# Kernel optimization log

Measured on AMD Instinct MI355X. Metric: run time of the kernel, lower is better.

Reference implementation:

```python
import jax, jax.numpy as jnp
import numpy as np

N = 200000
D_NODE = 256
D_EDGE = 128
D_OUT = 256
J = 17


def setup_inputs() -> dict:
    key = jax.random.key(0)
    ks = jax.random.split(key, 16)
    s = 0.02
    return {
        "nodes_1": jax.random.normal(ks[0], (N, D_NODE), jnp.float32),
        "nodes_2": jax.random.normal(ks[1], (N, D_NODE), jnp.float32),
        "edges": jax.random.normal(ks[2], (N, D_EDGE), jnp.float32),
        "node_types_1": jax.random.randint(ks[3], (N,), 0, J),
        "node_types_2": jax.random.randint(ks[4], (N,), 0, J),
        # per-joint linear stacks (torch Linear weight [out,in] stored transposed as [in,out])
        "W1": jax.random.normal(ks[5], (J, D_NODE, D_OUT), jnp.float32) * s,
        "b1": jax.random.normal(ks[6], (J, D_OUT), jnp.float32) * s,
        "W2": jax.random.normal(ks[7], (J, D_NODE, D_OUT), jnp.float32) * s,
        "b2": jax.random.normal(ks[8], (J, D_OUT), jnp.float32) * s,
        "We": jax.random.normal(ks[9], (D_EDGE, D_OUT), jnp.float32) * s,
        "be": jax.random.normal(ks[10], (D_OUT,), jnp.float32) * s,
        "Wout": jax.random.normal(ks[11], (3 * D_OUT, D_OUT), jnp.float32) * s,
        "bout": jax.random.normal(ks[12], (D_OUT,), jnp.float32) * s,
    }


def _per_type_linear(nodes, types, W, b):
    # Equivalent to: for each joint i, tmp[types==i] = nodes[types==i] @ W[i] + b[i]
    out = jnp.zeros((nodes.shape[0], W.shape[2]), nodes.dtype)
    for i in range(W.shape[0]):  # small fixed loop over joint types
        yi = nodes @ W[i] + b[i]
        out = jnp.where((types == i)[:, None], yi, out)
    return out


def reference(nodes_1, nodes_2, edges, node_types_1, node_types_2,
              W1, b1, W2, b2, We, be, Wout, bout):
    tmp_1 = _per_type_linear(nodes_1, node_types_1, W1, b1)
    tmp_2 = _per_type_linear(nodes_2, node_types_2, W2, b2)
    e = edges @ We + be
    cat = jnp.concatenate([tmp_1, tmp_2, e], axis=1)  # [N, 3*D_OUT]
    h = jax.nn.relu(cat) @ Wout + bout
    return jax.nn.relu(h)
```

## Files before the change

kernel.cpp:

```cpp
#include <hip/hip_runtime.h>


#define J_TYPES 17
#define PAIRS   (J_TYPES * J_TYPES)
#define DN      256
#define DE      128
#define DO      256
#define TILE    64
#define LDA     264
#define LDE     136

typedef short bf16x8 __attribute__((ext_vector_type(8)));
typedef float f32x4  __attribute__((ext_vector_type(4)));

#define BAR() asm volatile("s_waitcnt lgkmcnt(0)\n\ts_barrier" ::: "memory")

__device__ __forceinline__ unsigned short f2bf(float x) {
  unsigned u = __float_as_uint(x);
  return (unsigned short)((u + 0x7fffu + ((u >> 16) & 1u)) >> 16);
}

__device__ __forceinline__ unsigned cvtpk(float lo, float hi) {
  unsigned r;
  asm("v_cvt_pk_bf16_f32 %0, %1, %2" : "=v"(r) : "v"(lo), "v"(hi));
  return r;
}

__global__ void prep_w_k(const float* __restrict__ W1, const float* __restrict__ W2,
                         const float* __restrict__ We, const float* __restrict__ Wout,
                         unsigned short* __restrict__ W1t, unsigned short* __restrict__ W2t,
                         unsigned short* __restrict__ Wet, unsigned short* __restrict__ Ut) {
  const int SZW = J_TYPES * 65536;
  const int total = SZW * 2 + DE * DO + 3 * 65536;
  for (int o = blockIdx.x * blockDim.x + threadIdx.x; o < total;
       o += gridDim.x * blockDim.x) {
    int idx = o;
    if (idx < SZW) {
      int j = idx >> 16, r = idx & 65535;
      int i = r & 7, lane = (r >> 3) & 63, t = r >> 9;
      int k32 = t & 7, colt = t >> 3;
      int col = colt * 16 + (lane & 15);
      int k = k32 * 32 + ((lane >> 4) << 3) + i;
      W1t[idx] = f2bf(W1[((size_t)j * 256 + k) * 256 + col]);
    } else if ((idx -= SZW) < SZW) {
      int j = idx >> 16, r = idx & 65535;
      int i = r & 7, lane = (r >> 3) & 63, t = r >> 9;
      int k32 = t & 7, colt = t >> 3;
      int col = colt * 16 + (lane & 15);
      int k = k32 * 32 + ((lane >> 4) << 3) + i;
      W2t[idx] = f2bf(W2[((size_t)j * 256 + k) * 256 + col]);
    } else if ((idx -= SZW) < DE * DO) {
      int r = idx;
      int i = r & 7, lane = (r >> 3) & 63, t = r >> 9;
      int k32 = t & 3, colt = t >> 2;
      int col = colt * 16 + (lane & 15);
      int k = k32 * 32 + ((lane >> 4) << 3) + i;
      Wet[idx] = f2bf(We[(size_t)k * 256 + col]);
    } else {
      idx -= DE * DO;
      int p = idx >> 16, r = idx & 65535;
      int i = r & 7, lane = (r >> 3) & 63, t = r >> 9;
      int k32 = t & 7, colt = t >> 3;
      int col = colt * 16 + (lane & 15);
      int k = k32 * 32 + ((lane >> 4) << 3) + i;
      Ut[idx] = f2bf(Wout[((size_t)p * 256 + k) * 256 + col]);
    }
  }
}

__global__ void hist_k(const int* __restrict__ ty1, const int* __restrict__ ty2,
                       int* __restrict__ cnt, int N) {
  __shared__ int h[PAIRS];
  for (int i = threadIdx.x; i < PAIRS; i += blockDim.x) h[i] = 0;
  __syncthreads();
  for (int i = blockIdx.x * blockDim.x + threadIdx.x; i < N;
       i += gridDim.x * blockDim.x)
    atomicAdd(&h[ty1[i] * J_TYPES + ty2[i]], 1);
  __syncthreads();
  for (int i = threadIdx.x; i < PAIRS; i += blockDim.x) {
    int v = h[i];
    if (v) atomicAdd(&cnt[i], v);
  }
}

__global__ void scan_tiles_k(const int* __restrict__ cnt, int* __restrict__ seg,
                             int* __restrict__ tpair, int* __restrict__ tstart,
                             int* __restrict__ tnr, int* __restrict__ ntl) {
  __shared__ int s1[512], s2[512];
  int t = threadIdx.x;
  int c  = (t < PAIRS) ? cnt[t] : 0;
  int nt = (c + TILE - 1) / TILE;
  s1[t] = c; s2[t] = nt;
  __syncthreads();
  for (int o = 1; o < 512; o <<= 1) {
    int v1 = (t >= o) ? s1[t - o] : 0;
    int v2 = (t >= o) ? s2[t - o] : 0;
    __syncthreads();
    s1[t] += v1; s2[t] += v2;
    __syncthreads();
  }
  if (t < PAIRS) {
    int segstart = s1[t] - c;
    int tbase    = s2[t] - nt;
    seg[t] = segstart;
    for (int i = 0; i < nt; ++i) {
      tpair[tbase + i]  = t;
      tstart[tbase + i] = segstart + i * TILE;
      int rem = c - i * TILE;
      tnr[tbase + i] = rem < TILE ? rem : TILE;
    }
  }
  if (t == 511) ntl[0] = s2[511];
}

__global__ void scatter_k(const int* __restrict__ ty1, const int* __restrict__ ty2,
                          const int* __restrict__ seg, int* __restrict__ c2,
                          int* __restrict__ ridx, int N) {
  __shared__ int lh[PAIRS], lb[PAIRS];
  int chunk = (N + gridDim.x - 1) / gridDim.x;
  int lo = blockIdx.x * chunk;
  int hi = lo + chunk; if (hi > N) hi = N;
  for (int i = threadIdx.x; i < PAIRS; i += blockDim.x) lh[i] = 0;
  __syncthreads();
  for (int i = lo + threadIdx.x; i < hi; i += blockDim.x)
    atomicAdd(&lh[ty1[i] * J_TYPES + ty2[i]], 1);
  __syncthreads();
  for (int i = threadIdx.x; i < PAIRS; i += blockDim.x) {
    int v = lh[i];
    lb[i] = v ? atomicAdd(&c2[i], v) : 0;
    lh[i] = 0;
  }
  __syncthreads();
  for (int i = lo + threadIdx.x; i < hi; i += blockDim.x) {
    int p = ty1[i] * J_TYPES + ty2[i];
    int pos = seg[p] + lb[p] + atomicAdd(&lh[p], 1);
    ridx[pos] = i;
  }
}


__device__ __forceinline__ void stage256(const float* __restrict__ src,
                                         const int* __restrict__ ridxp, int nrows,
                                         unsigned short* lds, int wave, int lane) {
  float4 f[8];
#pragma unroll
  for (int j = 0; j < 8; ++j) {
    int r = wave + 8 * j;
    int rc = r < nrows ? r : nrows - 1;
    int sr = ridxp[rc];
    f[j] = reinterpret_cast<const float4*>(src + (size_t)sr * DN)[lane];
  }
#pragma unroll
  for (int j = 0; j < 8; ++j) {
    int r = wave + 8 * j;
    unsigned lo = cvtpk(f[j].x, f[j].y), hi = cvtpk(f[j].z, f[j].w);
    *reinterpret_cast<uint2*>(lds + r * LDA + lane * 4) = make_uint2(lo, hi);
  }
}

__device__ __forceinline__ void stage128(const float* __restrict__ src,
                                         const int* __restrict__ ridxp, int nrows,
                                         unsigned short* lds, int wave, int lane) {
  float2 f[8];
#pragma unroll
  for (int j = 0; j < 8; ++j) {
    int r = wave + 8 * j;
    int rc = r < nrows ? r : nrows - 1;
    int sr = ridxp[rc];
    f[j] = reinterpret_cast<const float2*>(src + (size_t)sr * DE)[lane];
  }
#pragma unroll
  for (int j = 0; j < 8; ++j) {
    int r = wave + 8 * j;
    *reinterpret_cast<unsigned*>(lds + r * LDE + lane * 2) = cvtpk(f[j].x, f[j].y);
  }
}

template <int NK, int LD>
__device__ __forceinline__ void gemm32(const unsigned short* lds,
                                       const unsigned short* __restrict__ Wbase,
                                       f32x4 acc[4][2], int r0, int kg, int lane,
                                       int wave) {
  const unsigned short* w = Wbase + ((size_t)(wave * 2) * NK) * 512 + lane * 8;
  const int kw = wave & (NK - 1);
  bf16x8 bf[2][2];
#pragma unroll
  for (int cs = 0; cs < 2; ++cs)
    bf[0][cs] = *reinterpret_cast<const bf16x8*>(w + ((size_t)cs * NK + kw) * 512);
#pragma unroll
  for (int i = 0; i < NK; ++i) {
    const int cur = i & 1, nxt = cur ^ 1;
    const int kk = (i + wave) & (NK - 1);
    if (i + 1 < NK) {
      const int kk1 = (i + 1 + wave) & (NK - 1);
#pragma unroll
      for (int cs = 0; cs < 2; ++cs)
        bf[nxt][cs] =
            *reinterpret_cast<const bf16x8*>(w + ((size_t)cs * NK + kk1) * 512);
    }
    bf16x8 af[4];
#pragma unroll
    for (int rs = 0; rs < 4; ++rs)
      af[rs] = *reinterpret_cast<const bf16x8*>(lds + (rs * 16 + r0) * LD + kk * 32 + kg);
    __builtin_amdgcn_s_setprio(1);
#pragma unroll
    for (int rs = 0; rs < 4; ++rs)
#pragma unroll
      for (int cs = 0; cs < 2; ++cs)
        acc[rs][cs] = __builtin_amdgcn_mfma_f32_16x16x32_bf16(af[rs], bf[cur][cs],
                                                              acc[rs][cs], 0, 0, 0);
    __builtin_amdgcn_s_setprio(0);
  }
}

__device__ __forceinline__ void epi32(f32x4 accT[4][2], const float* __restrict__ bias,
                                      unsigned short* ldsT, int r0, int rb, int wave) {
#pragma unroll
  for (int cs = 0; cs < 2; ++cs) {
    int col = wave * 32 + cs * 16 + r0;
    float b = bias[col];
#pragma unroll
    for (int rs = 0; rs < 4; ++rs) {
      float x0 = fmaxf(accT[rs][cs][0] + b, 0.f);
      float x1 = fmaxf(accT[rs][cs][1] + b, 0.f);
      float x2 = fmaxf(accT[rs][cs][2] + b, 0.f);
      float x3 = fmaxf(accT[rs][cs][3] + b, 0.f);
      unsigned w01 = cvtpk(x0, x1), w23 = cvtpk(x2, x3);
      int row = rs * 16 + rb;
      ldsT[(row + 0) * LDA + col] = (unsigned short)w01;
      ldsT[(row + 1) * LDA + col] = (unsigned short)(w01 >> 16);
      ldsT[(row + 2) * LDA + col] = (unsigned short)w23;
      ldsT[(row + 3) * LDA + col] = (unsigned short)(w23 >> 16);
    }
  }
}

#define ZERO42(A)                                                        \
  _Pragma("unroll") for (int a_ = 0; a_ < 4; ++a_) _Pragma("unroll")     \
      for (int b_ = 0; b_ < 2; ++b_) A[a_][b_] = (f32x4){0.f, 0.f, 0.f, 0.f};

__global__ __launch_bounds__(512, 4) void fused_k(
    const float* __restrict__ n1, const float* __restrict__ n2,
    const float* __restrict__ eg, const unsigned short* __restrict__ W1t,
    const unsigned short* __restrict__ W2t, const unsigned short* __restrict__ Wet,
    const unsigned short* __restrict__ Ut, const float* __restrict__ b1,
    const float* __restrict__ b2, const float* __restrict__ be,
    const float* __restrict__ bout, const int* __restrict__ ridx,
    const int* __restrict__ tpair, const int* __restrict__ tstart,
    const int* __restrict__ tnr, const int* __restrict__ ntl,
    float* __restrict__ out) {
  int nwg = gridDim.x, orig = blockIdx.x;
  int q = nwg >> 3, rr = nwg & 7, xc = orig & 7, sidx = orig >> 3;
  int tile = (xc < rr ? xc * (q + 1) : rr * (q + 1) + (xc - rr) * q) + sidx;
  if (tile >= ntl[0]) return;

  const int pr = tpair[tile];
  const int t1 = pr / J_TYPES, t2 = pr % J_TYPES;
  const int ts = tstart[tile];
  const int nrows = tnr[tile];
  const int* __restrict__ ridxp = ridx + ts;

  __shared__ unsigned short ldsA[TILE * LDA];
  __shared__ unsigned short ldsT[TILE * LDA];
  __shared__ int srow[TILE];

  const int lane = threadIdx.x & 63;
  const int wave = __builtin_amdgcn_readfirstlane(threadIdx.x >> 6);
  const int r0 = lane & 15;
  const int kg = (lane >> 4) * 8;
  const int rb = (lane >> 4) * 4;

  if (threadIdx.x < TILE)
    srow[threadIdx.x] = (threadIdx.x < nrows) ? ridxp[threadIdx.x] : -1;

  f32x4 accT[4][2], accO[4][2];

  stage256(n1, ridxp, nrows, ldsA, wave, lane);
  BAR();

  ZERO42(accT);
  gemm32<8, LDA>(ldsA, W1t + (size_t)t1 * 65536, accT, r0, kg, lane, wave);
  BAR();

  epi32(accT, b1 + t1 * 256, ldsT, r0, rb, wave);
  stage256(n2, ridxp, nrows, ldsA, wave, lane);
  BAR();

  ZERO42(accO);
  gemm32<8, LDA>(ldsT, Ut, accO, r0, kg, lane, wave);
  ZERO42(accT);
  gemm32<8, LDA>(ldsA, W2t + (size_t)t2 * 65536, accT, r0, kg, lane, wave);
  BAR();

  epi32(accT, b2 + t2 * 256, ldsT, r0, rb, wave);
  stage128(eg, ridxp, nrows, ldsA, wave, lane);
  BAR();

  gemm32<8, LDA>(ldsT, Ut + 65536, accO, r0, kg, lane, wave);
  ZERO42(accT);
  gemm32<4, LDE>(ldsA, Wet, accT, r0, kg, lane, wave);
  BAR();

  epi32(accT, be, ldsT, r0, rb, wave);
  BAR();

  gemm32<8, LDA>(ldsT, Ut + 2 * 65536, accO, r0, kg, lane, wave);

#pragma unroll
  for (int cs = 0; cs < 2; ++cs) {
    int col = wave * 32 + cs * 16 + r0;
    float bo = bout[col];
#pragma unroll
    for (int rs = 0; rs < 4; ++rs)
#pragma unroll
      for (int i = 0; i < 4; ++i) {
        int row = rs * 16 + rb + i;
        if (row < nrows) {
          float v = fmaxf(accO[rs][cs][i] + bo, 0.f);
          out[(size_t)srow[row] * 256 + col] = v;
        }
      }
  }
}

extern "C" void kernel_launch(void* const* d_in, const int* in_sizes, int n_in,
                              void* d_out, int out_size, void* d_ws, size_t ws_size,
                              hipStream_t stream) {
  const float* n1   = (const float*)d_in[0];
  const float* n2   = (const float*)d_in[1];
  const float* eg   = (const float*)d_in[2];
  const int*   ty1  = (const int*)d_in[3];
  const int*   ty2  = (const int*)d_in[4];
  const float* W1   = (const float*)d_in[5];
  const float* b1   = (const float*)d_in[6];
  const float* W2   = (const float*)d_in[7];
  const float* b2   = (const float*)d_in[8];
  const float* We   = (const float*)d_in[9];
  const float* be   = (const float*)d_in[10];
  const float* Wout = (const float*)d_in[11];
  const float* bout = (const float*)d_in[12];
  float* out = (float*)d_out;

  const int N = in_sizes[0] / DN;
  const int maxt = (N + TILE - 1) / TILE + PAIRS;

  char* ws = (char*)d_ws;
  size_t off = 0;
  auto take = [&](size_t bytes) -> char* {
    char* p = ws + off;
    off += (bytes + 255) & ~(size_t)255;
    return p;
  };
  int* cnt = (int*)take(PAIRS * 4);
  int* c2  = (int*)take(PAIRS * 4);
  int* ntl = (int*)take(4);
  int* seg = (int*)take((PAIRS + 1) * 4);
  int* tp  = (int*)take((size_t)maxt * 4);
  int* tst = (int*)take((size_t)maxt * 4);
  int* tnr = (int*)take((size_t)maxt * 4);
  int* ridx = (int*)take((size_t)N * 4);
  unsigned short* W1t = (unsigned short*)take((size_t)J_TYPES * 65536 * 2);
  unsigned short* W2t = (unsigned short*)take((size_t)J_TYPES * 65536 * 2);
  unsigned short* Wet = (unsigned short*)take((size_t)DE * DO * 2);
  unsigned short* Ut  = (unsigned short*)take((size_t)3 * 65536 * 2);
  (void)ws_size; (void)n_in; (void)out_size;

  hipMemsetAsync(cnt, 0, (size_t)((char*)seg - (char*)cnt), stream);
  prep_w_k<<<1024, 256, 0, stream>>>(W1, W2, We, Wout, W1t, W2t, Wet, Ut);
  hist_k<<<400, 256, 0, stream>>>(ty1, ty2, cnt, N);
  scan_tiles_k<<<1, 512, 0, stream>>>(cnt, seg, tp, tst, tnr, ntl);
  scatter_k<<<256, 256, 0, stream>>>(ty1, ty2, seg, c2, ridx, N);
  fused_k<<<maxt, 512, 0, stream>>>(n1, n2, eg, W1t, W2t, Wet, Ut, b1, b2, be, bout,
                                    ridx, tp, tst, tnr, ntl, out);
}
```

Before: 289.5 us.

## Double-buffer input staging and split tile across 16 waves with 16-column slices

Moves the fused kernel from 512 to 1024 threads, so each of 16 waves computes a 16-column output slice instead of a 32-column one. Input row gathers are split into issue and LDS-write phases, and ldsA is double-buffered so the next input's global loads are in flight during the current GEMM. This is meant to hide gather latency and raise wave-level parallelism. In exchange it adds LDS use per block (an extra 64x264 bf16 buffer) and pairs 1024-thread blocks with launch_bounds(1024,4), which may constrain registers and occupancy.

After: 669.8 us. 131% more time.

```diff
diff --git a/kernel.cpp b/kernel.cpp
--- a/kernel.cpp
+++ b/kernel.cpp
@@ -139,64 +139,65 @@
 }
 
 
-__device__ __forceinline__ void stage256(const float* __restrict__ src,
+__device__ __forceinline__ void issue256(const float* __restrict__ src,
                                          const int* __restrict__ ridxp, int nrows,
-                                         unsigned short* lds, int wave, int lane) {
-  float4 f[8];
-#pragma unroll
-  for (int j = 0; j < 8; ++j) {
-    int r = wave + 8 * j;
+                                         int wave, int lane, float4 f[4]) {
+#pragma unroll
+  for (int j = 0; j < 4; ++j) {
+    int r = wave + 16 * j;
     int rc = r < nrows ? r : nrows - 1;
     int sr = ridxp[rc];
     f[j] = reinterpret_cast<const float4*>(src + (size_t)sr * DN)[lane];
   }
-#pragma unroll
-  for (int j = 0; j < 8; ++j) {
-    int r = wave + 8 * j;
+}
+
+__device__ __forceinline__ void write256(const float4 f[4], unsigned short* lds,
+                                         int wave, int lane) {
+#pragma unroll
+  for (int j = 0; j < 4; ++j) {
+    int r = wave + 16 * j;
     unsigned lo = cvtpk(f[j].x, f[j].y), hi = cvtpk(f[j].z, f[j].w);
     *reinterpret_cast<uint2*>(lds + r * LDA + lane * 4) = make_uint2(lo, hi);
   }
 }
 
-__device__ __forceinline__ void stage128(const float* __restrict__ src,
+__device__ __forceinline__ void issue128(const float* __restrict__ src,
                                          const int* __restrict__ ridxp, int nrows,
-                                         unsigned short* lds, int wave, int lane) {
-  float2 f[8];
-#pragma unroll
-  for (int j = 0; j < 8; ++j) {
-    int r = wave + 8 * j;
+                                         int wave, int lane, float2 f[4]) {
+#pragma unroll
+  for (int j = 0; j < 4; ++j) {
+    int r = wave + 16 * j;
     int rc = r < nrows ? r : nrows - 1;
     int sr = ridxp[rc];
     f[j] = reinterpret_cast<const float2*>(src + (size_t)sr * DE)[lane];
   }
-#pragma unroll
-  for (int j = 0; j < 8; ++j) {
-    int r = wave + 8 * j;
+}
+
+__device__ __forceinline__ void write128(const float2 f[4], unsigned short* lds,
+                                         int wave, int lane) {
+#pragma unroll
+  for (int j = 0; j < 4; ++j) {
+    int r = wave + 16 * j;
     *reinterpret_cast<unsigned*>(lds + r * LDE + lane * 2) = cvtpk(f[j].x, f[j].y);
   }
 }
 
 template <int NK, int LD>
-__device__ __forceinline__ void gemm32(const unsigned short* lds,
+__device__ __forceinline__ void gemm16(const unsigned short* lds,
                                        const unsigned short* __restrict__ Wbase,
-                                       f32x4 acc[4][2], int r0, int kg, int lane,
+                                       f32x4 acc[4], int r0, int kg, int lane,
                                        int wave) {
-  const unsigned short* w = Wbase + ((size_t)(wave * 2) * NK) * 512 + lane * 8;
+  const unsigned short* w = Wbase + ((size_t)wave * NK) * 512 + lane * 8;
   const int kw = wave & (NK - 1);
-  bf16x8 bf[2][2];
-#pragma unroll
-  for (int cs = 0; cs < 2; ++cs)
-    bf[0][cs] = *reinterpret_cast<const bf16x8*>(w + ((size_t)cs * NK + kw) * 512);
+  bf16x8 bf[2];
+  bf[0] = *reinterpret_cast<const bf16x8*>(w + (size_t)kw * 512);
 #pragma unroll
   for (int i = 0; i < NK; ++i) {
     const int cur = i & 1, nxt = cur ^ 1;
     const int kk = (i + wave) & (NK - 1);
     if (i + 1 < NK) {
       const int kk1 = (i + 1 + wave) & (NK - 1);
-#pragma unroll
-      for (int cs = 0; cs < 2; ++cs)
-        bf[nxt][cs] =
-            *reinterpret_cast<const bf16x8*>(w + ((size_t)cs * NK + kk1) * 512);
+      bf[nxt] = *reinterpret_cast<const bf16x8*>(w + (size_t)kk1 * 512);
     }
     bf16x8 af[4];
 #pragma unroll
@@ -205,41 +206,36 @@
     __builtin_amdgcn_s_setprio(1);
 #pragma unroll
     for (int rs = 0; rs < 4; ++rs)
-#pragma unroll
-      for (int cs = 0; cs < 2; ++cs)
-        acc[rs][cs] = __builtin_amdgcn_mfma_f32_16x16x32_bf16(af[rs], bf[cur][cs],
-                                                              acc[rs][cs], 0, 0, 0);
+      acc[rs] = __builtin_amdgcn_mfma_f32_16x16x32_bf16(af[rs], bf[cur], acc[rs],
+                                                        0, 0, 0);
     __builtin_amdgcn_s_setprio(0);
   }
 }
 
-__device__ __forceinline__ void epi32(f32x4 accT[4][2], const float* __restrict__ bias,
+__device__ __forceinline__ void epi16(f32x4 accT[4], const float* __restrict__ bias,
                                       unsigned short* ldsT, int r0, int rb, int wave) {
-#pragma unroll
-  for (int cs = 0; cs < 2; ++cs) {
-    int col = wave * 32 + cs * 16 + r0;
-    float b = bias[col];
-#pragma unroll
-    for (int rs = 0; rs < 4; ++rs) {
-      float x0 = fmaxf(accT[rs][cs][0] + b, 0.f);
-      float x1 = fmaxf(accT[rs][cs][1] + b, 0.f);
-      float x2 = fmaxf(accT[rs][cs][2] + b, 0.f);
-      float x3 = fmaxf(accT[rs][cs][3] + b, 0.f);
-      unsigned w01 = cvtpk(x0, x1), w23 = cvtpk(x2, x3);
-      int row = rs * 16 + rb;
-      ldsT[(row + 0) * LDA + col] = (unsigned short)w01;
-      ldsT[(row + 1) * LDA + col] = (unsigned short)(w01 >> 16);
-      ldsT[(row + 2) * LDA + col] = (unsigned short)w23;
-      ldsT[(row + 3) * LDA + col] = (unsigned short)(w23 >> 16);
-    }
-  }
-}
-
-#define ZERO42(A)                                                        \
-  _Pragma("unroll") for (int a_ = 0; a_ < 4; ++a_) _Pragma("unroll")     \
-      for (int b_ = 0; b_ < 2; ++b_) A[a_][b_] = (f32x4){0.f, 0.f, 0.f, 0.f};
-
-__global__ __launch_bounds__(512, 4) void fused_k(
+  const int col = wave * 16 + r0;
+  const float b = bias[col];
+#pragma unroll
+  for (int rs = 0; rs < 4; ++rs) {
+    float x0 = fmaxf(accT[rs][0] + b, 0.f);
+    float x1 = fmaxf(accT[rs][1] + b, 0.f);
+    float x2 = fmaxf(accT[rs][2] + b, 0.f);
+    float x3 = fmaxf(accT[rs][3] + b, 0.f);
+    unsigned w01 = cvtpk(x0, x1), w23 = cvtpk(x2, x3);
+    int row = rs * 16 + rb;
+    ldsT[(row + 0) * LDA + col] = (unsigned short)w01;
+    ldsT[(row + 1) * LDA + col] = (unsigned short)(w01 >> 16);
+    ldsT[(row + 2) * LDA + col] = (unsigned short)w23;
+    ldsT[(row + 3) * LDA + col] = (unsigned short)(w23 >> 16);
+  }
+}
+
+#define ZERO4(A)                                                         \
+  _Pragma("unroll") for (int a_ = 0; a_ < 4; ++a_)                       \
+      A[a_] = (f32x4){0.f, 0.f, 0.f, 0.f};
+
+__global__ __launch_bounds__(1024, 4) void fused_k(
     const float* __restrict__ n1, const float* __restrict__ n2,
     const float* __restrict__ eg, const unsigned short* __restrict__ W1t,
     const unsigned short* __restrict__ W2t, const unsigned short* __restrict__ Wet,
@@ -260,7 +256,7 @@
   const int nrows = tnr[tile];
   const int* __restrict__ ridxp = ridx + ts;
 
-  __shared__ unsigned short ldsA[TILE * LDA];
+  __shared__ unsigned short ldsA[2][TILE * LDA];
   __shared__ unsigned short ldsT[TILE * LDA];
   __shared__ int srow[TILE];
 
@@ -273,50 +269,54 @@
   if (threadIdx.x < TILE)
     srow[threadIdx.x] = (threadIdx.x < nrows) ? ridxp[threadIdx.x] : -1;
 
-  f32x4 accT[4][2], accO[4][2];
-
-  stage256(n1, ridxp, nrows, ldsA, wave, lane);
-  BAR();
-
-  ZERO42(accT);
-  gemm32<8, LDA>(ldsA, W1t + (size_t)t1 * 65536, accT, r0, kg, lane, wave);
-  BAR();
-
-  epi32(accT, b1 + t1 * 256, ldsT, r0, rb, wave);
-  stage256(n2, ridxp, nrows, ldsA, wave, lane);
-  BAR();
-
-  ZERO42(accO);
-  gemm32<8, LDA>(ldsT, Ut, accO, r0, kg, lane, wave);
-  ZERO42(accT);
-  gemm32<8, LDA>(ldsA, W2t + (size_t)t2 * 65536, accT, r0, kg, lane, wave);
-  BAR();
-
-  epi32(accT, b2 + t2 * 256, ldsT, r0, rb, wave);
-  stage128(eg, ridxp, nrows, ldsA, wave, lane);
-  BAR();
-
-  gemm32<8, LDA>(ldsT, Ut + 65536, accO, r0, kg, lane, wave);
-  ZERO42(accT);
-  gemm32<4, LDE>(ldsA, Wet, accT, r0, kg, lane, wave);
-  BAR();
-
-  epi32(accT, be, ldsT, r0, rb, wave);
-  BAR();
-
-  gemm32<8, LDA>(ldsT, Ut + 2 * 65536, accO, r0, kg, lane, wave);
-
-#pragma unroll
-  for (int cs = 0; cs < 2; ++cs) {
-    int col = wave * 32 + cs * 16 + r0;
-    float bo = bout[col];
+  f32x4 accT[4], accO[4];
+  float4 f4[4];
+  float2 f2[4];
+
+  issue256(n1, ridxp, nrows, wave, lane, f4);
+  write256(f4, ldsA[0], wave, lane);
+  BAR();
+
+  issue256(n2, ridxp, nrows, wave, lane, f4);
+  ZERO4(accT);
+  gemm16<8, LDA>(ldsA[0], W1t + (size_t)t1 * 65536, accT, r0, kg, lane, wave);
+  write256(f4, ldsA[1], wave, lane);
+  BAR();
+
+  epi16(accT, b1 + t1 * 256, ldsT, r0, rb, wave);
+  BAR();
+
+  issue128(eg, ridxp, nrows, wave, lane, f2);
+  ZERO4(accO);
+  gemm16<8, LDA>(ldsT, Ut, accO, r0, kg, lane, wave);
+  ZERO4(accT);
+  gemm16<8, LDA>(ldsA[1], W2t + (size_t)t2 * 65536, accT, r0, kg, lane, wave);
+  write128(f2, ldsA[0], wave, lane);
+  BAR();
+
+  epi16(accT, b2 + t2 * 256, ldsT, r0, rb, wave);
+  BAR();
+
+  gemm16<8, LDA>(ldsT, Ut + 65536, accO, r0, kg, lane, wave);
+  ZERO4(accT);
+  gemm16<4, LDE>(ldsA[0], Wet, accT, r0, kg, lane, wave);
+  BAR();
+
+  epi16(accT, be, ldsT, r0, rb, wave);
+  BAR();
+
+  gemm16<8, LDA>(ldsT, Ut + 2 * 65536, accO, r0, kg, lane, wave);
+
+  {
+    const int col = wave * 16 + r0;
+    const float bo = bout[col];
 #pragma unroll
     for (int rs = 0; rs < 4; ++rs)
 #pragma unroll
       for (int i = 0; i < 4; ++i) {
         int row = rs * 16 + rb + i;
         if (row < nrows) {
-          float v = fmaxf(accO[rs][cs][i] + bo, 0.f);
+          float v = fmaxf(accO[rs][i] + bo, 0.f);
           out[(size_t)srow[row] * 256 + col] = v;
         }
       }
@@ -370,6 +370,6 @@
   hist_k<<<400, 256, 0, stream>>>(ty1, ty2, cnt, N);
   scan_tiles_k<<<1, 512, 0, stream>>>(cnt, seg, tp, tst, tnr, ntl);
   scatter_k<<<256, 256, 0, stream>>>(ty1, ty2, seg, c2, ridx, N);
-  fused_k<<<maxt, 512, 0, stream>>>(n1, n2, eg, W1t, W2t, Wet, Ut, b1, b2, be, bout,
-                                    ridx, tp, tst, tnr, ntl, out);
-}
+  fused_k<<<maxt, 1024, 0, stream>>>(n1, n2, eg, W1t, W2t, Wet, Ut, b1, b2, be, bout,
+                                     ridx, tp, tst, tnr, ntl, out);
+}
```
